# Performance work log

Measured on AMD Instinct MI355X. Metric: run time of the kernel, lower is better.

## Reference

```python
import jax, jax.numpy as jnp
import numpy as np

N_NODES = 100000
N_EDGES = 2000000
EPS = 1e-8


def setup_inputs() -> dict:
    key = jax.random.key(0)
    k1, k2 = jax.random.split(key)
    node_positions = jax.random.normal(k1, (1, N_NODES, 2), dtype=jnp.float32) * 10.0
    adjacency = jnp.zeros((1, 1, 1), dtype=jnp.float32)  # unused by this axiom
    edge_index = jax.random.randint(k2, (2, N_EDGES), 0, N_NODES, dtype=jnp.int32)
    return {"node_positions": node_positions, "adjacency": adjacency, "edge_index": edge_index}


def reference(node_positions, adjacency, edge_index):
    """OrthogonalIntegrityAxiom loss.

    Mathematically identical to enumerating all intra-node edge pairs (i<j)
    and averaging cos^2(theta)*(1-cos^2(theta)) = dot^2 - dot^4 over pairs.
    Uses the moment identity: per node n with incident unit directions d_i,
      sum_{i,j} (d_i.d_j)^2 = ||sum_i d_i (x) d_i||_F^2
      sum_{i,j} (d_i.d_j)^4 = ||sum_i d_i^{(x)4}||_F^2
    Diagonal (i=j) terms equal 1 in both sums and cancel in the difference,
    so sum_{i<j} (dot^2 - dot^4) = (S2_n - S4_n)/2.
    """
    pos = node_positions.reshape(-1, 2)                      # (N, 2)
    n_total = pos.shape[0]
    src, dst = edge_index[0], edge_index[1]
    d = pos[dst] - pos[src]                                  # (E, 2)
    d = d / jnp.maximum(jnp.linalg.norm(d, axis=-1, keepdims=True), EPS)

    # Each edge is incident to both endpoints -> 2E (node, direction) pairs.
    nodes = jnp.concatenate([src, dst])                      # (2E,)
    dirs = jnp.concatenate([d, d], axis=0)                   # (2E, 2)

    o2 = (dirs[:, :, None] * dirs[:, None, :]).reshape(-1, 4)    # d (x) d, (2E, 4)
    o4 = (o2[:, :, None] * o2[:, None, :]).reshape(-1, 16)       # d^{(x)4}, (2E, 16)

    M = jax.ops.segment_sum(o2, nodes, num_segments=n_total)     # (N, 4)
    T = jax.ops.segment_sum(o4, nodes, num_segments=n_total)     # (N, 16)
    deg = jax.ops.segment_sum(jnp.ones_like(dirs[:, 0]), nodes, num_segments=n_total)

    S2 = jnp.sum(M * M, axis=-1)   # per-node sum_{i,j} (d_i.d_j)^2
    S4 = jnp.sum(T * T, axis=-1)   # per-node sum_{i,j} (d_i.d_j)^4

    pair_loss_sum = 0.5 * jnp.sum(S2 - S4)
    n_pairs = 0.5 * jnp.sum(deg * (deg - 1.0))
    loss = pair_loss_sum / jnp.maximum(n_pairs, 1.0)
    return loss
```

## Files before the change

kernel.cpp:

```cpp
#include <hip/hip_runtime.h>
#include <math.h>

#define EPSV 1e-8f

static constexpr double QC = 1.0 / 1024.0;
static constexpr double QS = 1.0 / 512.0;

static constexpr int BLOG = 8;
static constexpr int NPB = 1 << BLOG;
static constexpr int NBIN = 512;
static constexpr int SRTN = 8192;
static constexpr int NODE_BLOCKS = 256;

__device__ __forceinline__ unsigned int make_record(float dx, float dy) {
    float n2 = dx * dx + dy * dy;
    if (n2 > EPSV * EPSV) {
        float inv = 1.0f / n2;
        float c2 = (dx * dx - dy * dy) * inv;
        float s2 = (2.0f * dx * dy) * inv;
        float c4 = c2 * c2 - s2 * s2;
        float s4 = 2.0f * c2 * s2;
        c4 = fminf(fmaxf(c4, -1.0f), 1.0f);
        s4 = fminf(fmaxf(s4, -1.0f), 1.0f);
        unsigned int c4q = (unsigned int)__float2int_rn((c4 + 1.0f) * 1024.0f);
        unsigned int s4q = (unsigned int)__float2int_rn((s4 + 1.0f) * 512.0f);
        return (c4q << 11) | s4q;
    }
    return (1u << 31) | (1024u << 11) | 512u;
}

__device__ __forceinline__ unsigned long long rec_to_val(unsigned int r) {
    return (((unsigned long long)(r >> 31)) << 60) | (1ull << 52)
         | (((unsigned long long)((r >> 11) & 0xFFFu)) << 26)
         | (unsigned long long)(r & 0x7FFu);
}

__device__ __forceinline__ void decode_accum(unsigned long long a, double& pls, double& npr) {
    double s4sum = (double)(a & 0x3FFFFFFull);
    double c4sum = (double)((a >> 26) & 0x3FFFFFFull);
    double deg = (double)((a >> 52) & 0xFFull);
    double z = (double)(a >> 60);
    double u = deg - z;
    double C = c4sum * QC - deg;
    double S = s4sum * QS - deg;
    pls += (u * u - C * C - S * S) * 0.0625;
    npr += 0.5 * deg * (deg - 1.0);
}

__global__ __launch_bounds__(256) void bin_kernel(
    const float2* __restrict__ pos,
    const int* __restrict__ ei,
    int E, int NB, int chunk, int rstride,
    unsigned short* __restrict__ ofs_out,
    unsigned int* __restrict__ buf)
{
    __shared__ unsigned int srt[SRTN];
    __shared__ unsigned int hist[512];
    __shared__ unsigned int scan[512];
    int blk = blockIdx.x;
    int t = threadIdx.x;
    int e0 = blk * chunk;
    int e1 = min(E, e0 + chunk);
    int cl = max(0, e1 - e0);
    const int* src = ei;
    const int* dst = ei + E;

    hist[t] = 0; hist[t + 256] = 0;
    __syncthreads();
    for (int e = e0 + t; e < e1; e += 256) {
        atomicAdd(&hist[src[e] >> BLOG], 1u);
        atomicAdd(&hist[dst[e] >> BLOG], 1u);
    }
    __syncthreads();
    scan[t] = hist[t]; scan[t + 256] = hist[t + 256];
    __syncthreads();
    for (int d = 1; d < 512; d <<= 1) {
        unsigned a0 = scan[t] + ((t >= d) ? scan[t - d] : 0u);
        int t2 = t + 256;
        unsigned a1 = scan[t2] + ((t2 >= d) ? scan[t2 - d] : 0u);
        __syncthreads();
        scan[t] = a0; scan[t2] = a1;
        __syncthreads();
    }
    unsigned ex0 = scan[t] - hist[t];
    unsigned ex1 = scan[t + 256] - hist[t + 256];
    size_t row = (size_t)blk * (size_t)(NB + 1);
    if (t < NB) ofs_out[row + t] = (unsigned short)ex0;
    if (t + 256 < NB) ofs_out[row + t + 256] = (unsigned short)ex1;
    if (t == 0) ofs_out[row + NB] = (unsigned short)(2 * cl);
    __syncthreads();
    hist[t] = ex0; hist[t + 256] = ex1;
    __syncthreads();
    for (int e = e0 + t; e < e1; e += 256) {
        int s = src[e], d = dst[e];
        float2 ps = pos[s], pd = pos[d];
        unsigned int rec = make_record(pd.x - ps.x, pd.y - ps.y);
        unsigned is = atomicAdd(&hist[s >> BLOG], 1u);
        srt[is] = rec | ((unsigned)(s & (NPB - 1)) << 23);
        unsigned it = atomicAdd(&hist[d >> BLOG], 1u);
        srt[it] = rec | ((unsigned)(d & (NPB - 1)) << 23);
    }
    __syncthreads();
    unsigned int* dstb = buf + (size_t)blk * (size_t)rstride;
    int nrec = 2 * cl;
    for (int i = t; i < nrec; i += 256) dstb[i] = srt[i];
}

__global__ __launch_bounds__(256) void bucket_kernel(
    const unsigned int* __restrict__ buf,
    const unsigned short* __restrict__ ofs,
    int rstride, int NB, int nbin,
    double* __restrict__ partials)
{
    __shared__ unsigned long long acc[4][NPB];
    __shared__ double sha[4], shb[4];
    int b = blockIdx.x;
    int t = threadIdx.x;
    int wid = t >> 6;
    for (int i = t; i < 4 * NPB; i += 256)
        ((unsigned long long*)acc)[i] = 0ull;
    __syncthreads();

    for (int run = t; run < nbin; run += 256) {
        size_t row = (size_t)run * (size_t)(NB + 1);
        unsigned o0 = ofs[row + b];
        unsigned o1 = ofs[row + b + 1];
        const unsigned int* p = buf + (size_t)run * (size_t)rstride + o0;
        for (unsigned i = 0; i < o1 - o0; ++i) {
            unsigned r = p[i];
            unsigned id = (r >> 23) & (NPB - 1);
            atomicAdd(&acc[wid][id], rec_to_val(r));
        }
    }
    __syncthreads();

    double pls = 0.0, npr = 0.0;
    for (int i = t; i < NPB; i += 256) {
        unsigned long long a = acc[0][i] + acc[1][i] + acc[2][i] + acc[3][i];
        decode_accum(a, pls, npr);
    }
    for (int off = 32; off > 0; off >>= 1) {
        pls += __shfl_down(pls, off, 64);
        npr += __shfl_down(npr, off, 64);
    }
    int lane = t & 63;
    if (lane == 0) { sha[wid] = pls; shb[wid] = npr; }
    __syncthreads();
    if (t == 0) {
        partials[2 * b + 0] = sha[0] + sha[1] + sha[2] + sha[3];
        partials[2 * b + 1] = shb[0] + shb[1] + shb[2] + shb[3];
    }
}

__global__ __launch_bounds__(256) void final_kernel(
    const double* __restrict__ partials,
    float* __restrict__ out,
    int nb)
{
    double pls = 0.0, npr = 0.0;
    for (int i = threadIdx.x; i < nb; i += blockDim.x) {
        pls += partials[2 * i + 0];
        npr += partials[2 * i + 1];
    }
    __shared__ double sha[4], shb[4];
    for (int off = 32; off > 0; off >>= 1) {
        pls += __shfl_down(pls, off, 64);
        npr += __shfl_down(npr, off, 64);
    }
    int lane = threadIdx.x & 63;
    int wid = threadIdx.x >> 6;
    if (lane == 0) { sha[wid] = pls; shb[wid] = npr; }
    __syncthreads();
    if (threadIdx.x == 0) {
        double a = sha[0] + sha[1] + sha[2] + sha[3];
        double b = shb[0] + shb[1] + shb[2] + shb[3];
        out[0] = (float)(a / fmax(b, 1.0));
    }
}

__global__ __launch_bounds__(256) void edge_kernel_fb(
    const float2* __restrict__ pos,
    const int* __restrict__ ei,
    unsigned long long* __restrict__ acc,
    int E)
{
    int tid = blockIdx.x * blockDim.x + threadIdx.x;
    int nthreads = gridDim.x * blockDim.x;
    const int* src = ei;
    const int* dst = ei + E;
    for (int e = tid; e < E; e += nthreads) {
        int s = src[e], t = dst[e];
        float2 ps = pos[s], pt = pos[t];
        unsigned long long val = rec_to_val(make_record(pt.x - ps.x, pt.y - ps.y));
        atomicAdd(&acc[s], val);
        atomicAdd(&acc[t], val);
    }
}

__global__ __launch_bounds__(256) void node_kernel_fb(
    const unsigned long long* __restrict__ acc,
    double* __restrict__ partials,
    int N)
{
    int tid = blockIdx.x * blockDim.x + threadIdx.x;
    int nthreads = gridDim.x * blockDim.x;
    double pls = 0.0, npr = 0.0;
    for (int n = tid; n < N; n += nthreads)
        decode_accum(acc[n], pls, npr);
    __shared__ double sha[4], shb[4];
    for (int off = 32; off > 0; off >>= 1) {
        pls += __shfl_down(pls, off, 64);
        npr += __shfl_down(npr, off, 64);
    }
    int lane = threadIdx.x & 63;
    int wid = threadIdx.x >> 6;
    if (lane == 0) { sha[wid] = pls; shb[wid] = npr; }
    __syncthreads();
    if (threadIdx.x == 0) {
        partials[2 * blockIdx.x + 0] = sha[0] + sha[1] + sha[2] + sha[3];
        partials[2 * blockIdx.x + 1] = shb[0] + shb[1] + shb[2] + shb[3];
    }
}

extern "C" void kernel_launch(void* const* d_in, const int* in_sizes, int n_in,
                              void* d_out, int out_size, void* d_ws, size_t ws_size,
                              hipStream_t stream) {
    const float* pos = (const float*)d_in[0];
    const int* ei = (const int*)d_in[2];
    int N = in_sizes[0] / 2;
    int E = in_sizes[2] / 2;
    float* out = (float*)d_out;

    int NB = (N + NPB - 1) >> BLOG;
    int chunk = (E + NBIN - 1) / NBIN;
    int nrec_max = 2 * chunk;
    int rstride = (nrec_max + 15) & ~15;

    size_t off_buf = (size_t)NB * 16;
    size_t off_ofs = off_buf + (size_t)NBIN * (size_t)rstride * 4;
    size_t need = off_ofs + (size_t)NBIN * (size_t)(NB + 1) * 2;

    if (ws_size >= need && nrec_max <= SRTN && NB + 1 <= 512 && nrec_max < 65536) {
        double* partials = (double*)d_ws;
        unsigned int* buf = (unsigned int*)((char*)d_ws + off_buf);
        unsigned short* ofs = (unsigned short*)((char*)d_ws + off_ofs);

        bin_kernel<<<NBIN, 256, 0, stream>>>(
            (const float2*)pos, ei, E, NB, chunk, rstride, ofs, buf);
        bucket_kernel<<<NB, 256, 0, stream>>>(buf, ofs, rstride, NB, NBIN, partials);
        final_kernel<<<1, 256, 0, stream>>>(partials, out, NB);
    } else {
        unsigned long long* acc = (unsigned long long*)d_ws;
        double* partials = (double*)((char*)d_ws + (size_t)N * 8);
        hipMemsetAsync(d_ws, 0, (size_t)N * 8 + (size_t)NODE_BLOCKS * 16, stream);
        int eb = min((E + 255) / 256, 2048);
        edge_kernel_fb<<<eb, 256, 0, stream>>>((const float2*)pos, ei, acc, E);
        node_kernel_fb<<<NODE_BLOCKS, 256, 0, stream>>>(acc, partials, N);
        final_kernel<<<1, 256, 0, stream>>>(partials, out, NODE_BLOCKS);
    }
}
```

Before: 115.5 us.

## Replace two-pass binning with per-XCD privatized global atomic accumulation

Drops the sort/bin kernel and the bucket kernel, which staged packed edge records through global memory. Each edge now adds its packed record directly into a per-node 64-bit accumulator with a global atomic. The accumulator array is replicated once per XCD, chosen by reading the hardware XCC ID, so atomics stay within one XCD's L2 and can use workgroup memory scope. A node kernel then sums the 8 replicas and reduces. The costs are a memset of 8×N accumulators, 4M scattered global atomics, and reliance on XCC-ID routing and weak-scope atomics for correctness.

```diff
diff --git a/kernel.cpp b/kernel.cpp
--- a/kernel.cpp
+++ b/kernel.cpp
@@ -6,11 +6,8 @@
 static constexpr double QC = 1.0 / 1024.0;
 static constexpr double QS = 1.0 / 512.0;
 
-static constexpr int BLOG = 8;
-static constexpr int NPB = 1 << BLOG;
-static constexpr int NBIN = 512;
-static constexpr int SRTN = 8192;
 static constexpr int NODE_BLOCKS = 256;
+static constexpr int NXCD = 8;
 
 __device__ __forceinline__ unsigned int make_record(float dx, float dy) {
     float n2 = dx * dx + dy * dy;
@@ -47,108 +44,69 @@
     npr += 0.5 * deg * (deg - 1.0);
 }
 
-__global__ __launch_bounds__(256) void bin_kernel(
+__device__ __forceinline__ void do_edge(const float2* __restrict__ pos,
+                                        unsigned long long* __restrict__ acc,
+                                        int s, int d) {
+    float2 ps = pos[s], pt = pos[d];
+    unsigned long long v = rec_to_val(make_record(pt.x - ps.x, pt.y - ps.y));
+    __hip_atomic_fetch_add(&acc[s], v, __ATOMIC_RELAXED, __HIP_MEMORY_SCOPE_WORKGROUP);
+    __hip_atomic_fetch_add(&acc[d], v, __ATOMIC_RELAXED, __HIP_MEMORY_SCOPE_WORKGROUP);
+}
+
+__global__ __launch_bounds__(256) void edge_kernel_xcd(
     const float2* __restrict__ pos,
     const int* __restrict__ ei,
-    int E, int NB, int chunk, int rstride,
-    unsigned short* __restrict__ ofs_out,
-    unsigned int* __restrict__ buf)
-{
-    __shared__ unsigned int srt[SRTN];
-    __shared__ unsigned int hist[512];
-    __shared__ unsigned int scan[512];
-    int blk = blockIdx.x;
-    int t = threadIdx.x;
-    int e0 = blk * chunk;
-    int e1 = min(E, e0 + chunk);
-    int cl = max(0, e1 - e0);
+    unsigned long long* __restrict__ accs,
+    int N, int E)
+{
+    unsigned int xcc;
+    asm volatile("s_getreg_b32 %0, hwreg(HW_REG_XCC_ID)" : "=s"(xcc));
+    unsigned long long* __restrict__ acc =
+        accs + (size_t)(xcc & (NXCD - 1)) * (size_t)N;
     const int* src = ei;
     const int* dst = ei + E;
-
-    hist[t] = 0; hist[t + 256] = 0;
-    __syncthreads();
-    for (int e = e0 + t; e < e1; e += 256) {
-        atomicAdd(&hist[src[e] >> BLOG], 1u);
-        atomicAdd(&hist[dst[e] >> BLOG], 1u);
-    }
-    __syncthreads();
-    scan[t] = hist[t]; scan[t + 256] = hist[t + 256];
-    __syncthreads();
-    for (int d = 1; d < 512; d <<= 1) {
-        unsigned a0 = scan[t] + ((t >= d) ? scan[t - d] : 0u);
-        int t2 = t + 256;
-        unsigned a1 = scan[t2] + ((t2 >= d) ? scan[t2 - d] : 0u);
-        __syncthreads();
-        scan[t] = a0; scan[t2] = a1;
-        __syncthreads();
-    }
-    unsigned ex0 = scan[t] - hist[t];
-    unsigned ex1 = scan[t + 256] - hist[t + 256];
-    size_t row = (size_t)blk * (size_t)(NB + 1);
-    if (t < NB) ofs_out[row + t] = (unsigned short)ex0;
-    if (t + 256 < NB) ofs_out[row + t + 256] = (unsigned short)ex1;
-    if (t == 0) ofs_out[row + NB] = (unsigned short)(2 * cl);
-    __syncthreads();
-    hist[t] = ex0; hist[t + 256] = ex1;
-    __syncthreads();
-    for (int e = e0 + t; e < e1; e += 256) {
-        int s = src[e], d = dst[e];
-        float2 ps = pos[s], pd = pos[d];
-        unsigned int rec = make_record(pd.x - ps.x, pd.y - ps.y);
-        unsigned is = atomicAdd(&hist[s >> BLOG], 1u);
-        srt[is] = rec | ((unsigned)(s & (NPB - 1)) << 23);
-        unsigned it = atomicAdd(&hist[d >> BLOG], 1u);
-        srt[it] = rec | ((unsigned)(d & (NPB - 1)) << 23);
-    }
-    __syncthreads();
-    unsigned int* dstb = buf + (size_t)blk * (size_t)rstride;
-    int nrec = 2 * cl;
-    for (int i = t; i < nrec; i += 256) dstb[i] = srt[i];
-}
-
-__global__ __launch_bounds__(256) void bucket_kernel(
-    const unsigned int* __restrict__ buf,
-    const unsigned short* __restrict__ ofs,
-    int rstride, int NB, int nbin,
-    double* __restrict__ partials)
-{
-    __shared__ unsigned long long acc[4][NPB];
+    int tid = blockIdx.x * blockDim.x + threadIdx.x;
+    int nth = gridDim.x * blockDim.x;
+    int nq = E >> 2;
+    for (int q = tid; q < nq; q += nth) {
+        int4 s4 = ((const int4*)src)[q];
+        int4 d4 = ((const int4*)dst)[q];
+        do_edge(pos, acc, s4.x, d4.x);
+        do_edge(pos, acc, s4.y, d4.y);
+        do_edge(pos, acc, s4.z, d4.z);
+        do_edge(pos, acc, s4.w, d4.w);
+    }
+    for (int e = (nq << 2) + tid; e < E; e += nth)
+        do_edge(pos, acc, src[e], dst[e]);
+}
+
+__global__ __launch_bounds__(256) void node_kernel_xcd(
+    const unsigned long long* __restrict__ accs,
+    double* __restrict__ partials,
+    int N)
+{
+    int tid = blockIdx.x * blockDim.x + threadIdx.x;
+    int nth = gridDim.x * blockDim.x;
+    double pls = 0.0, npr = 0.0;
+    for (int n = tid; n < N; n += nth) {
+        unsigned long long a = 0ull;
+        #pragma unroll
+        for (int r = 0; r < NXCD; ++r)
+            a += accs[(size_t)r * (size_t)N + n];
+        decode_accum(a, pls, npr);
+    }
     __shared__ double sha[4], shb[4];
-    int b = blockIdx.x;
-    int t = threadIdx.x;
-    int wid = t >> 6;
-    for (int i = t; i < 4 * NPB; i += 256)
-        ((unsigned long long*)acc)[i] = 0ull;
-    __syncthreads();
-
-    for (int run = t; run < nbin; run += 256) {
-        size_t row = (size_t)run * (size_t)(NB + 1);
-        unsigned o0 = ofs[row + b];
-        unsigned o1 = ofs[row + b + 1];
-        const unsigned int* p = buf + (size_t)run * (size_t)rstride + o0;
-        for (unsigned i = 0; i < o1 - o0; ++i) {
-            unsigned r = p[i];
-            unsigned id = (r >> 23) & (NPB - 1);
-            atomicAdd(&acc[wid][id], rec_to_val(r));
-        }
-    }
-    __syncthreads();
-
-    double pls = 0.0, npr = 0.0;
-    for (int i = t; i < NPB; i += 256) {
-        unsigned long long a = acc[0][i] + acc[1][i] + acc[2][i] + acc[3][i];
-        decode_accum(a, pls, npr);
-    }
     for (int off = 32; off > 0; off >>= 1) {
         pls += __shfl_down(pls, off, 64);
         npr += __shfl_down(npr, off, 64);
     }
-    int lane = t & 63;
+    int lane = threadIdx.x & 63;
+    int wid = threadIdx.x >> 6;
     if (lane == 0) { sha[wid] = pls; shb[wid] = npr; }
     __syncthreads();
-    if (t == 0) {
-        partials[2 * b + 0] = sha[0] + sha[1] + sha[2] + sha[3];
-        partials[2 * b + 1] = shb[0] + shb[1] + shb[2] + shb[3];
+    if (threadIdx.x == 0) {
+        partials[2 * blockIdx.x + 0] = sha[0] + sha[1] + sha[2] + sha[3];
+        partials[2 * blockIdx.x + 1] = shb[0] + shb[1] + shb[2] + shb[3];
     }
 }
 
@@ -231,24 +189,21 @@
     int E = in_sizes[2] / 2;
     float* out = (float*)d_out;
 
-    int NB = (N + NPB - 1) >> BLOG;
-    int chunk = (E + NBIN - 1) / NBIN;
-    int nrec_max = 2 * chunk;
-    int rstride = (nrec_max + 15) & ~15;
-
-    size_t off_buf = (size_t)NB * 16;
-    size_t off_ofs = off_buf + (size_t)NBIN * (size_t)rstride * 4;
-    size_t need = off_ofs + (size_t)NBIN * (size_t)(NB + 1) * 2;
-
-    if (ws_size >= need && nrec_max <= SRTN && NB + 1 <= 512 && nrec_max < 65536) {
-        double* partials = (double*)d_ws;
-        unsigned int* buf = (unsigned int*)((char*)d_ws + off_buf);
-        unsigned short* ofs = (unsigned short*)((char*)d_ws + off_ofs);
-
-        bin_kernel<<<NBIN, 256, 0, stream>>>(
-            (const float2*)pos, ei, E, NB, chunk, rstride, ofs, buf);
-        bucket_kernel<<<NB, 256, 0, stream>>>(buf, ofs, rstride, NB, NBIN, partials);
-        final_kernel<<<1, 256, 0, stream>>>(partials, out, NB);
+    size_t acc_bytes = (size_t)NXCD * (size_t)N * 8;
+    size_t need = acc_bytes + (size_t)NODE_BLOCKS * 16;
+
+    if (ws_size >= need) {
+        unsigned long long* accs = (unsigned long long*)d_ws;
+        double* partials = (double*)((char*)d_ws + acc_bytes);
+        hipMemsetAsync(d_ws, 0, acc_bytes, stream);
+        int nq = E >> 2;
+        int eb = (nq + 255) / 256;
+        if (eb < 1) eb = 1;
+        if (eb > 8192) eb = 8192;
+        edge_kernel_xcd<<<eb, 256, 0, stream>>>(
+            (const float2*)pos, ei, accs, N, E);
+        node_kernel_xcd<<<NODE_BLOCKS, 256, 0, stream>>>(accs, partials, N);
+        final_kernel<<<1, 256, 0, stream>>>(partials, out, NODE_BLOCKS);
     } else {
         unsigned long long* acc = (unsigned long long*)d_ws;
         double* partials = (double*)((char*)d_ws + (size_t)N * 8);
```

Result: slower. 249.9 us (+116.3%).
